# Kernel tuning notes

Hardware: AMD Instinct MI355X
Metric: run time of the kernel (lower is better)

## Reference

```python
import jax, jax.numpy as jnp
import numpy as np

B, T, F = 2, 128, 88          # batch, time frames, pitch bins (hard-coded 88)
HIDDEN = 64                    # LSTM input dim
N_UNIT = 64                    # channel dim (= 2 * lstm hidden 32)
N_HEAD = 4
HEAD_DIM = N_UNIT // N_HEAD    # 16
WINDOW = 7
N_LAYERS = 2
DIFF_STEPS = 100
LSTM_H = N_UNIT // 2           # 32 per direction


def setup_inputs() -> dict:
    key = jax.random.key(0)
    ks = jax.random.split(key, 12)
    s = 0.05
    inp = {
        'x': jax.random.normal(ks[0], (B, T * F, HIDDEN), jnp.float32),
        't': jax.random.randint(ks[1], (B,), 0, DIFF_STEPS, jnp.int32),
        # LSTM params, stacked [layer, direction, ...]; layer-1 input dim == 2*LSTM_H == HIDDEN
        'lstm_w_ih': s * jax.random.normal(ks[2], (N_LAYERS, 2, 4 * LSTM_H, HIDDEN), jnp.float32),
        'lstm_w_hh': s * jax.random.normal(ks[3], (N_LAYERS, 2, 4 * LSTM_H, LSTM_H), jnp.float32),
        'lstm_b_ih': s * jax.random.normal(ks[4], (N_LAYERS, 2, 4 * LSTM_H), jnp.float32),
        'lstm_b_hh': s * jax.random.normal(ks[5], (N_LAYERS, 2, 4 * LSTM_H), jnp.float32),
        # per-NA-layer params
        't_emb': s * jax.random.normal(ks[6], (N_LAYERS, DIFF_STEPS, N_UNIT), jnp.float32),
        'w_qkv': s * jax.random.normal(ks[7], (N_LAYERS, N_UNIT, 3 * N_UNIT), jnp.float32),
        'b_qkv': jnp.zeros((N_LAYERS, 3 * N_UNIT), jnp.float32),
        'rpb': s * jax.random.normal(ks[8], (N_LAYERS, N_HEAD, 2 * WINDOW - 1, 2 * WINDOW - 1), jnp.float32),
        'w_proj': s * jax.random.normal(ks[9], (N_LAYERS, N_UNIT, N_UNIT), jnp.float32),
        'b_proj': jnp.zeros((N_LAYERS, N_UNIT), jnp.float32),
    }
    return inp


def _lstm_dir(x, w_ih, w_hh, b_ih, b_hh, reverse):
    # x: [N, T, D]; pytorch gate order i, f, g, o
    N = x.shape[0]
    H = w_hh.shape[1]
    xs = jnp.swapaxes(x, 0, 1)
    if reverse:
        xs = xs[::-1]
    b = b_ih + b_hh
    def step(carry, xt):
        h, c = carry
        g = xt @ w_ih.T + h @ w_hh.T + b
        i, f, gg, o = jnp.split(g, 4, axis=-1)
        c = jax.nn.sigmoid(f) * c + jax.nn.sigmoid(i) * jnp.tanh(gg)
        h = jax.nn.sigmoid(o) * jnp.tanh(c)
        return (h, c), h
    h0 = jnp.zeros((N, H), x.dtype)
    _, hs = jax.lax.scan(step, (h0, h0), xs)
    if reverse:
        hs = hs[::-1]
    return jnp.swapaxes(hs, 0, 1)


def _bilstm(x, w_ih, w_hh, b_ih, b_hh):
    for l in range(w_ih.shape[0]):
        fwd = _lstm_dir(x, w_ih[l, 0], w_hh[l, 0], b_ih[l, 0], b_hh[l, 0], False)
        bwd = _lstm_dir(x, w_ih[l, 1], w_hh[l, 1], b_ih[l, 1], b_hh[l, 1], True)
        x = jnp.concatenate([fwd, bwd], axis=-1)
    return x


def _nbh(L, w):
    # NATTEN-style clamped (non-shrinking) neighborhood window per axis
    i = jnp.arange(L)
    start = jnp.clip(i - w // 2, 0, L - w)
    idx = start[:, None] + jnp.arange(w)[None, :]   # [L, w] absolute neighbor idx
    rel = idx - i[:, None] + (w - 1)                # [L, w] rel-pos-bias idx in [0, 2w-2]
    return idx, rel


def _na2d(x, t_idx, emb, wqkv, bqkv, rpb_l, wproj, bproj):
    # x: [B, Th, Tw, C]; diffusion-step conditioning via learned embedding add
    Bx, Th, Tw, C = x.shape
    h = x + emb[t_idx][:, None, None, :]
    qkv = (h @ wqkv + bqkv).reshape(Bx, Th, Tw, 3, N_HEAD, HEAD_DIM)
    q = jnp.moveaxis(qkv[..., 0, :, :], 3, 1) * (HEAD_DIM ** -0.5)  # [B,h,Th,Tw,d]
    k = jnp.moveaxis(qkv[..., 1, :, :], 3, 1)
    v = jnp.moveaxis(qkv[..., 2, :, :], 3, 1)
    ih, rh = _nbh(Th, WINDOW)
    iw, rw = _nbh(Tw, WINDOW)
    # gather windowed neighbors: [B,h,Th,Tw,w,w,d]
    kn = k[:, :, ih[:, None, :, None], iw[None, :, None, :], :]
    vn = v[:, :, ih[:, None, :, None], iw[None, :, None, :], :]
    bias = rpb_l[:, rh[:, None, :, None], rw[None, :, None, :]]     # [h,Th,Tw,w,w]
    logits = jnp.einsum('bhijd,bhijkld->bhijkl', q, kn) + bias[None]
    attn = jax.nn.softmax(logits.reshape(Bx, N_HEAD, Th, Tw, -1), axis=-1).reshape(logits.shape)
    out = jnp.einsum('bhijkl,bhijkld->bhijd', attn, vn)             # [B,h,Th,Tw,d]
    out = jnp.moveaxis(out, 1, 3).reshape(Bx, Th, Tw, C)
    return out @ wproj + bproj


def reference(x, t, lstm_w_ih, lstm_w_hh, lstm_b_ih, lstm_b_hh,
              t_emb, w_qkv, b_qkv, rpb, w_proj, b_proj):
    Bx = x.shape[0]
    Hin = x.shape[-1]
    Tt = x.shape[1] // F
    h = x.reshape(Bx, Tt, F, Hin).transpose(0, 2, 1, 3).reshape(Bx * F, Tt, Hin)
    h = _bilstm(h, lstm_w_ih, lstm_w_hh, lstm_b_ih, lstm_b_hh)      # [B*88, T, n_unit]
    # -> [B, T, 88, n_unit] 2D grid (height=T, width=88)
    h = h.reshape(Bx, F, Tt, N_UNIT).transpose(0, 2, 1, 3)
    for l in range(N_LAYERS):
        h = h + _na2d(h, t, t_emb[l], w_qkv[l], b_qkv[l], rpb[l], w_proj[l], b_proj[l])
    return h
```

## Files before the change

kernel.cpp:

```cpp
#include <hip/hip_runtime.h>
#include <math.h>

#define B_ 2
#define T_ 128
#define F_ 88
#define HID 64
#define NU 64
#define NH 4
#define HD 16
#define LH 32
#define NSEQ (B_*F_)
#define NTOK (B_*T_*F_)
#define NPOS (T_*F_)

__device__ __forceinline__ float fsig(float x) {
    return __builtin_amdgcn_rcpf(1.0f + __expf(-x));
}
__device__ __forceinline__ float ftanh(float x) {
    return 2.0f * __builtin_amdgcn_rcpf(1.0f + __expf(-2.0f*x)) - 1.0f;
}
__device__ __forceinline__ float rdlane(float v, int l) {
    return __uint_as_float(__builtin_amdgcn_readlane(__float_as_uint(v), l));
}

template<int LAYER>
__global__ void __launch_bounds__(256, 2) gg_kernel(
    const float* __restrict__ xin,
    const float* __restrict__ w_ih,
    const float* __restrict__ b_ih,
    const float* __restrict__ b_hh,
    float* __restrict__ G)
{
    __shared__ __align__(16) float xts[32][68];
    __shared__ __align__(16) float wsh[256][68];
    __shared__ float bsh[256];
    const int s  = blockIdx.x;
    const int t0 = blockIdx.y * 32;
    const int b = s / F_, f = s % F_;
    const int tid = threadIdx.x;

    for (int n = tid; n < 32*64; n += 256) {
        const int tt = n >> 6, k = n & 63;
        xts[tt][k] = (LAYER == 0)
            ? xin[(((size_t)b*T_ + t0+tt)*F_ + f)*HID + k]
            : xin[((size_t)s*T_ + t0+tt)*HID + k];
    }
    for (int n = tid; n < 256*64; n += 256) {
        const int row = n >> 6, k = n & 63;
        wsh[row][k] = w_ih[((size_t)LAYER*256 + row)*HID + k];
    }
    bsh[tid] = b_ih[LAYER*256 + tid] + b_hh[LAYER*256 + tid];
    __syncthreads();

    const int lane = tid & 63;
    const int g    = tid >> 6;
    const int dir  = g >> 1;
    const int th   = g & 1;
    const int rowA = dir*128 + lane;
    const int rowB = dir*128 + 64 + lane;

    float accA[16] = {}, accB[16] = {};
    #pragma unroll 4
    for (int k4 = 0; k4 < 16; k4++) {
        const float4 wA = *(const float4*)&wsh[rowA][k4*4];
        const float4 wB = *(const float4*)&wsh[rowB][k4*4];
        #pragma unroll
        for (int tt = 0; tt < 16; tt++) {
            const float4 xv = *(const float4*)&xts[th*16+tt][k4*4];
            accA[tt] += wA.x*xv.x + wA.y*xv.y + wA.z*xv.z + wA.w*xv.w;
            accB[tt] += wB.x*xv.x + wB.y*xv.y + wB.z*xv.z + wB.w*xv.w;
        }
    }
    const float bA = bsh[rowA], bB = bsh[rowB];
    float2* gout = (float2*)G + ((size_t)(s*2+dir)*T_ + t0 + th*16)*64 + lane;
    #pragma unroll
    for (int tt = 0; tt < 16; tt++) {
        float2 o; o.x = accA[tt] + bA; o.y = accB[tt] + bB;
        gout[(size_t)tt*64] = o;
    }
}

template<int LAYER>
__global__ void __launch_bounds__(128, 1) lstm_rec(
    const float* __restrict__ G,
    const float* __restrict__ w_hh,
    float* __restrict__ outp)
{
    const int s = blockIdx.x;
    const int b = s / F_, f = s % F_;
    const int lane = threadIdx.x & 63;
    const int dir  = threadIdx.x >> 6;

    float whA[LH], whB[LH];
    {
        const float4* pa = (const float4*)(w_hh + ((size_t)(LAYER*2+dir)*128 + lane)*LH);
        const float4* pb = (const float4*)(w_hh + ((size_t)(LAYER*2+dir)*128 + 64 + lane)*LH);
        #pragma unroll
        for (int k4 = 0; k4 < LH/4; k4++) {
            float4 a = pa[k4], c4 = pb[k4];
            whA[k4*4+0]=a.x;  whA[k4*4+1]=a.y;  whA[k4*4+2]=a.z;  whA[k4*4+3]=a.w;
            whB[k4*4+0]=c4.x; whB[k4*4+1]=c4.y; whB[k4*4+2]=c4.z; whB[k4*4+3]=c4.w;
        }
    }
    const float2* gp = (const float2*)G + (size_t)(s*2+dir)*T_*64 + lane;
    #define GTIME(st) (dir ? (T_-1-(st)) : (st))

    float h = 0.f, c = 0.f;

    #define STEP(gAv, gBv, stepi)                                            \
    {                                                                        \
        float aA0 = (gAv), aB0 = (gBv), aA1 = 0.f, aB1 = 0.f;                \
        _Pragma("unroll")                                                    \
        for (int k = 0; k < 16; k++) {                                       \
            const float hk  = rdlane(h, k);                                  \
            const float hk2 = rdlane(h, k+16);                               \
            aA0 += whA[k]*hk;     aB0 += whB[k]*hk;                          \
            aA1 += whA[k+16]*hk2; aB1 += whB[k+16]*hk2;                      \
        }                                                                    \
        const float accA = aA0 + aA1, accB = aB0 + aB1;                      \
        const float e0 = fsig(accA);                                         \
        const float e1 = (lane < LH) ? ftanh(accB) : fsig(accB);             \
        const float x0 = __shfl_xor(e0, 32, 64);       \
        const float x1 = __shfl_xor(e1, 32, 64);       \
        c = x0*c + e0*e1;                                                    \
        h = x1 * ftanh(c);                                                   \
        if (lane < LH) {                                                     \
            const int tm = GTIME(stepi);                                     \
            if (LAYER == 0)                                                  \
                outp[((size_t)s*T_ + tm)*NU + dir*LH + lane] = h;            \
            else                                                             \
                outp[(((size_t)b*T_ + tm)*F_ + f)*NU + dir*LH + lane] = h;   \
        }                                                                    \
    }

    float2 A[4], Bf[4];
    #pragma unroll
    for (int i = 0; i < 4; i++) A[i]  = gp[(size_t)GTIME(i)*64];
    #pragma unroll
    for (int i = 0; i < 4; i++) Bf[i] = gp[(size_t)GTIME(4+i)*64];

    #pragma unroll 1
    for (int grp = 0; grp < 32; grp++) {
        float2 P[4];
        const int pf = (grp < 30 ? grp + 2 : 31) * 4;
        #pragma unroll
        for (int i = 0; i < 4; i++) P[i] = gp[(size_t)GTIME(pf+i)*64];
        #pragma unroll
        for (int i = 0; i < 4; i++) { STEP(A[i].x, A[i].y, grp*4 + i); }
        #pragma unroll
        for (int i = 0; i < 4; i++) { A[i] = Bf[i]; Bf[i] = P[i]; }
    }
    #undef STEP
    #undef GTIME
}

__global__ void __launch_bounds__(256, 2) qkv_kernel(
    const float* __restrict__ hcur,
    const int*   __restrict__ tarr,
    const float* __restrict__ t_emb,
    const float* __restrict__ w_qkv,
    const float* __restrict__ b_qkv,
    const int layer,
    float* __restrict__ qb, float* __restrict__ kb, float* __restrict__ vb)
{
    __shared__ float as[64][65];
    __shared__ float wsh[64][64];
    const int m0 = blockIdx.x * 64;
    const int which = blockIdx.y;
    const int tid = threadIdx.x;
    const int bidx = m0 / NPOS;
    const int tb = tarr[bidx];
    const float* embp = t_emb + ((size_t)layer*100 + tb)*HID;

    for (int n = tid; n < 64*64; n += 256) {
        const int mm = n >> 6, k = n & 63;
        as[mm][k]  = hcur[((size_t)m0+mm)*64 + k] + embp[k];
        wsh[mm][k] = w_qkv[((size_t)layer*64 + mm)*192 + which*64 + k];
    }
    __syncthreads();

    const int tm = tid >> 4, tn = tid & 15;
    float acc[4][4] = {};
    for (int k = 0; k < 64; k++) {
        const float a0 = as[tm*4+0][k];
        const float a1 = as[tm*4+1][k];
        const float a2 = as[tm*4+2][k];
        const float a3 = as[tm*4+3][k];
        const float4 w = *(const float4*)&wsh[k][tn*4];
        acc[0][0]+=a0*w.x; acc[0][1]+=a0*w.y; acc[0][2]+=a0*w.z; acc[0][3]+=a0*w.w;
        acc[1][0]+=a1*w.x; acc[1][1]+=a1*w.y; acc[1][2]+=a1*w.z; acc[1][3]+=a1*w.w;
        acc[2][0]+=a2*w.x; acc[2][1]+=a2*w.y; acc[2][2]+=a2*w.z; acc[2][3]+=a2*w.w;
        acc[3][0]+=a3*w.x; acc[3][1]+=a3*w.y; acc[3][2]+=a3*w.z; acc[3][3]+=a3*w.w;
    }

    float* dst = (which == 0) ? qb : (which == 1) ? kb : vb;
    const float scale = (which == 0) ? 0.25f : 1.0f;
    const int hh = tn >> 2;
    const int dbase = (tn & 3) * 4;
    const float4 bv = *(const float4*)&b_qkv[(size_t)layer*192 + which*64 + tn*4];
    #pragma unroll
    for (int r = 0; r < 4; r++) {
        const int row = m0 + tm*4 + r;
        const int pos = row - bidx*NPOS;
        float4 o;
        o.x = (acc[r][0] + bv.x) * scale;
        o.y = (acc[r][1] + bv.y) * scale;
        o.z = (acc[r][2] + bv.z) * scale;
        o.w = (acc[r][3] + bv.w) * scale;
        *(float4*)&dst[(((size_t)bidx*NH + hh)*NPOS + pos)*HD + dbase] = o;
    }
}

__global__ void __launch_bounds__(192, 1) nattn_kernel(
    const float* __restrict__ qb,
    const float* __restrict__ kb,
    const float* __restrict__ vb,
    const float* __restrict__ rpb,
    const int layer,
    float* __restrict__ ao)
{
    __shared__ float ks[8][88][20];
    __shared__ float rp[169];
    const int blk = blockIdx.x;
    const int bh = blk & 7;
    const int it = blk >> 3;
    const int i0 = it*2;
    const int h  = bh & 3;
    const int bb = bh >> 2;
    const int tid = threadIdx.x;
    const int rs = min(max(i0-3, 0), T_-8);
    const float* kbase = kb + (size_t)bh*NPOS*HD;
    const float* vbase = vb + (size_t)bh*NPOS*HD;

    const bool act = (tid < 2*F_);
    const int isub = act ? (tid / F_) : 0;
    const int j    = act ? (tid - isub*F_) : 0;
    const int i    = i0 + isub;
    const int ihs  = min(max(i-3, 0), T_-7);
    const int ro   = ihs - rs;
    const int cw   = min(max(j-3, 0), F_-7);

    float4 q0, q1, q2, q3;
    if (act) {
        const float4* qp = (const float4*)&qb[((size_t)bh*NPOS + i*F_ + j)*HD];
        q0 = qp[0]; q1 = qp[1]; q2 = qp[2]; q3 = qp[3];
    }
    for (int n = tid; n < 169; n += 192)
        rp[n] = rpb[((size_t)layer*NH + h)*169 + n];
    for (int n4 = tid; n4 < 8*88*4; n4 += 192) {
        const int d4   = n4 & 3;
        const int rest = n4 >> 2;
        const int c    = rest % 88;
        const int r    = rest / 88;
        *(float4*)&ks[r][c][d4*4] =
            *(const float4*)&kbase[((size_t)(rs+r)*F_ + c)*HD + d4*4];
    }
    __syncthreads();

    float lg[49];
    if (act) {
        #pragma unroll
        for (int ki = 0; ki < 7; ki++) {
            const int rh = ihs + ki - i + 6;
            #pragma unroll
            for (int kj = 0; kj < 7; kj++) {
                const float4* kp = (const float4*)&ks[ro+ki][cw+kj][0];
                const float4 k0 = kp[0], k1 = kp[1], k2 = kp[2], k3 = kp[3];
                float d = q0.x*k0.x + q0.y*k0.y + q0.z*k0.z + q0.w*k0.w
                        + q1.x*k1.x + q1.y*k1.y + q1.z*k1.z + q1.w*k1.w
                        + q2.x*k2.x + q2.y*k2.y + q2.z*k2.z + q2.w*k2.w
                        + q3.x*k3.x + q3.y*k3.y + q3.z*k3.z + q3.w*k3.w;
                lg[ki*7+kj] = d + rp[rh*13 + (cw + kj - j + 6)];
            }
        }
        float m = lg[0];
        #pragma unroll
        for (int n = 1; n < 49; n++) m = fmaxf(m, lg[n]);
        float ssum = 0.f;
        #pragma unroll
        for (int n = 0; n < 49; n++) { lg[n] = __expf(lg[n] - m); ssum += lg[n]; }
        const float inv = __builtin_amdgcn_rcpf(ssum);
        #pragma unroll
        for (int n = 0; n < 49; n++) lg[n] *= inv;
    }
    __syncthreads();
    for (int n4 = tid; n4 < 8*88*4; n4 += 192) {
        const int d4   = n4 & 3;
        const int rest = n4 >> 2;
        const int c    = rest % 88;
        const int r    = rest / 88;
        *(float4*)&ks[r][c][d4*4] =
            *(const float4*)&vbase[((size_t)(rs+r)*F_ + c)*HD + d4*4];
    }
    __syncthreads();
    if (act) {
        float4 o0 = {0,0,0,0}, o1 = {0,0,0,0}, o2 = {0,0,0,0}, o3 = {0,0,0,0};
        #pragma unroll
        for (int ki = 0; ki < 7; ki++) {
            #pragma unroll
            for (int kj = 0; kj < 7; kj++) {
                const float a = lg[ki*7+kj];
                const float4* vp = (const float4*)&ks[ro+ki][cw+kj][0];
                const float4 v0 = vp[0], v1 = vp[1], v2 = vp[2], v3 = vp[3];
                o0.x += a*v0.x; o0.y += a*v0.y; o0.z += a*v0.z; o0.w += a*v0.w;
                o1.x += a*v1.x; o1.y += a*v1.y; o1.z += a*v1.z; o1.w += a*v1.w;
                o2.x += a*v2.x; o2.y += a*v2.y; o2.z += a*v2.z; o2.w += a*v2.w;
                o3.x += a*v3.x; o3.y += a*v3.y; o3.z += a*v3.z; o3.w += a*v3.w;
            }
        }
        float4* op = (float4*)&ao[(((size_t)bb*T_ + i)*F_ + j)*NU + h*HD];
        op[0]=o0; op[1]=o1; op[2]=o2; op[3]=o3;
    }
}

__global__ void __launch_bounds__(256, 2) proj_kernel(
    const float* __restrict__ ain,
    const float* __restrict__ hres,
    const float* __restrict__ w_proj,
    const float* __restrict__ b_proj,
    const int layer,
    float* __restrict__ outp)
{
    __shared__ float as[64][65];
    __shared__ float wsh[64][64];
    const int m0 = blockIdx.x * 64;
    const int tid = threadIdx.x;
    for (int n = tid; n < 64*64; n += 256) {
        const int mm = n >> 6, k = n & 63;
        as[mm][k]  = ain[((size_t)m0+mm)*64 + k];
        wsh[mm][k] = w_proj[(size_t)layer*4096 + n];
    }
    __syncthreads();
    const int tm = tid >> 4, tn = tid & 15;
    float acc[4][4] = {};
    for (int k = 0; k < 64; k++) {
        const float a0 = as[tm*4+0][k];
        const float a1 = as[tm*4+1][k];
        const float a2 = as[tm*4+2][k];
        const float a3 = as[tm*4+3][k];
        const float4 w = *(const float4*)&wsh[k][tn*4];
        acc[0][0]+=a0*w.x; acc[0][1]+=a0*w.y; acc[0][2]+=a0*w.z; acc[0][3]+=a0*w.w;
        acc[1][0]+=a1*w.x; acc[1][1]+=a1*w.y; acc[1][2]+=a1*w.z; acc[1][3]+=a1*w.w;
        acc[2][0]+=a2*w.x; acc[2][1]+=a2*w.y; acc[2][2]+=a2*w.z; acc[2][3]+=a2*w.w;
        acc[3][0]+=a3*w.x; acc[3][1]+=a3*w.y; acc[3][2]+=a3*w.z; acc[3][3]+=a3*w.w;
    }
    const float4 bv = *(const float4*)&b_proj[(size_t)layer*64 + tn*4];
    #pragma unroll
    for (int r = 0; r < 4; r++) {
        const int row = m0 + tm*4 + r;
        const float4 hv = *(const float4*)&hres[(size_t)row*64 + tn*4];
        float4 o;
        o.x = hv.x + acc[r][0] + bv.x;
        o.y = hv.y + acc[r][1] + bv.y;
        o.z = hv.z + acc[r][2] + bv.z;
        o.w = hv.w + acc[r][3] + bv.w;
        *(float4*)&outp[(size_t)row*64 + tn*4] = o;
    }
}

extern "C" void kernel_launch(void* const* d_in, const int* in_sizes, int n_in,
                              void* d_out, int out_size, void* d_ws, size_t ws_size,
                              hipStream_t stream) {
    const float* x      = (const float*)d_in[0];
    const int*   tarr   = (const int*)  d_in[1];
    const float* w_ih   = (const float*)d_in[2];
    const float* w_hh   = (const float*)d_in[3];
    const float* b_ih   = (const float*)d_in[4];
    const float* b_hh   = (const float*)d_in[5];
    const float* t_emb  = (const float*)d_in[6];
    const float* w_qkv  = (const float*)d_in[7];
    const float* b_qkv  = (const float*)d_in[8];
    const float* rpb    = (const float*)d_in[9];
    const float* w_proj = (const float*)d_in[10];
    const float* b_proj = (const float*)d_in[11];

    float* ws   = (float*)d_ws;
    const size_t CH = (size_t)NTOK * NU;
    float* hcur = ws;
    float* h0   = ws + CH;
    float* G    = ws + 2*CH;
    float* qbuf = ws + 2*CH;
    float* kbuf = ws + 3*CH;
    float* vbuf = ws + 4*CH;
    float* ao   = ws + 5*CH;
    float* outp = (float*)d_out;

    gg_kernel<0><<<dim3(NSEQ, T_/32), 256, 0, stream>>>(x,  w_ih, b_ih, b_hh, G);
    lstm_rec<0><<<NSEQ, 128, 0, stream>>>(G, w_hh, h0);
    gg_kernel<1><<<dim3(NSEQ, T_/32), 256, 0, stream>>>(h0, w_ih, b_ih, b_hh, G);
    lstm_rec<1><<<NSEQ, 128, 0, stream>>>(G, w_hh, hcur);

    for (int l = 0; l < 2; l++) {
        qkv_kernel<<<dim3(NTOK/64, 3), 256, 0, stream>>>(
            hcur, tarr, t_emb, w_qkv, b_qkv, l, qbuf, kbuf, vbuf);
        nattn_kernel<<<(T_/2)*8, 192, 0, stream>>>(
            qbuf, kbuf, vbuf, rpb, l, ao);
        proj_kernel<<<NTOK/64, 256, 0, stream>>>(
            ao, hcur, w_proj, b_proj, l, (l == 0) ? hcur : outp);
    }
}
```

Before: 266.4 us.

## Split LSTM directions into separate blocks and stage gate inputs in LDS

```diff
diff --git a/kernel.cpp b/kernel.cpp
--- a/kernel.cpp
+++ b/kernel.cpp
@@ -81,76 +81,80 @@
 }
 
 template<int LAYER>
-__global__ void __launch_bounds__(128, 1) lstm_rec(
+__global__ void __launch_bounds__(64, 1) lstm_rec(
     const float* __restrict__ G,
     const float* __restrict__ w_hh,
     float* __restrict__ outp)
 {
-    const int s = blockIdx.x;
+    __shared__ float2 gsl[T_][64];
+    const int s   = blockIdx.x >> 1;
+    const int dir = blockIdx.x & 1;
     const int b = s / F_, f = s % F_;
-    const int lane = threadIdx.x & 63;
-    const int dir  = threadIdx.x >> 6;
-
-    float whA[LH], whB[LH];
+    const int lane = threadIdx.x;
+
+    float2 wh2[LH];
     {
         const float4* pa = (const float4*)(w_hh + ((size_t)(LAYER*2+dir)*128 + lane)*LH);
         const float4* pb = (const float4*)(w_hh + ((size_t)(LAYER*2+dir)*128 + 64 + lane)*LH);
         #pragma unroll
         for (int k4 = 0; k4 < LH/4; k4++) {
             float4 a = pa[k4], c4 = pb[k4];
-            whA[k4*4+0]=a.x;  whA[k4*4+1]=a.y;  whA[k4*4+2]=a.z;  whA[k4*4+3]=a.w;
-            whB[k4*4+0]=c4.x; whB[k4*4+1]=c4.y; whB[k4*4+2]=c4.z; whB[k4*4+3]=c4.w;
-        }
-    }
-    const float2* gp = (const float2*)G + (size_t)(s*2+dir)*T_*64 + lane;
+            wh2[k4*4+0].x=a.x; wh2[k4*4+0].y=c4.x;
+            wh2[k4*4+1].x=a.y; wh2[k4*4+1].y=c4.y;
+            wh2[k4*4+2].x=a.z; wh2[k4*4+2].y=c4.z;
+            wh2[k4*4+3].x=a.w; wh2[k4*4+3].y=c4.w;
+        }
+    }
+
+    {
+        const float4* g4 = (const float4*)(G + (size_t)(s*2+dir)*T_*128);
+        float4* ls4 = (float4*)&gsl[0][0];
+        #pragma unroll 8
+        for (int it = 0; it < 64; it++)
+            ls4[it*64 + lane] = g4[(size_t)it*64 + lane];
+    }
+    __syncthreads();
+
+    const float a1 = (lane < LH) ? 2.f : 1.f;
+    const float c1 = (lane < LH) ? -1.f : 0.f;
+
+    float h = 0.f, c = 0.f;
     #define GTIME(st) (dir ? (T_-1-(st)) : (st))
 
-    float h = 0.f, c = 0.f;
-
-    #define STEP(gAv, gBv, stepi)                                            \
-    {                                                                        \
-        float aA0 = (gAv), aB0 = (gBv), aA1 = 0.f, aB1 = 0.f;                \
-        _Pragma("unroll")                                                    \
-        for (int k = 0; k < 16; k++) {                                       \
-            const float hk  = rdlane(h, k);                                  \
-            const float hk2 = rdlane(h, k+16);                               \
-            aA0 += whA[k]*hk;     aB0 += whB[k]*hk;                          \
-            aA1 += whA[k+16]*hk2; aB1 += whB[k+16]*hk2;                      \
-        }                                                                    \
-        const float accA = aA0 + aA1, accB = aB0 + aB1;                      \
-        const float e0 = fsig(accA);                                         \
-        const float e1 = (lane < LH) ? ftanh(accB) : fsig(accB);             \
-        const float x0 = __shfl_xor(e0, 32, 64);       \
-        const float x1 = __shfl_xor(e1, 32, 64);       \
-        c = x0*c + e0*e1;                                                    \
-        h = x1 * ftanh(c);                                                   \
-        if (lane < LH) {                                                     \
-            const int tm = GTIME(stepi);                                     \
-            if (LAYER == 0)                                                  \
-                outp[((size_t)s*T_ + tm)*NU + dir*LH + lane] = h;            \
-            else                                                             \
-                outp[(((size_t)b*T_ + tm)*F_ + f)*NU + dir*LH + lane] = h;   \
-        }                                                                    \
-    }
-
-    float2 A[4], Bf[4];
-    #pragma unroll
-    for (int i = 0; i < 4; i++) A[i]  = gp[(size_t)GTIME(i)*64];
-    #pragma unroll
-    for (int i = 0; i < 4; i++) Bf[i] = gp[(size_t)GTIME(4+i)*64];
-
-    #pragma unroll 1
-    for (int grp = 0; grp < 32; grp++) {
-        float2 P[4];
-        const int pf = (grp < 30 ? grp + 2 : 31) * 4;
-        #pragma unroll
-        for (int i = 0; i < 4; i++) P[i] = gp[(size_t)GTIME(pf+i)*64];
-        #pragma unroll
-        for (int i = 0; i < 4; i++) { STEP(A[i].x, A[i].y, grp*4 + i); }
-        #pragma unroll
-        for (int i = 0; i < 4; i++) { A[i] = Bf[i]; Bf[i] = P[i]; }
-    }
-    #undef STEP
+    float2 gcur = gsl[GTIME(0)][lane];
+    float2 gnxt = gsl[GTIME(1)][lane];
+
+    #pragma unroll 4
+    for (int step = 0; step < T_; step++) {
+        const int pf = step + 2 < T_ ? step + 2 : T_ - 1;
+        const float2 gpf = gsl[GTIME(pf)][lane];
+
+        float2 acc0 = gcur, acc1 = {0.f, 0.f};
+        #pragma unroll
+        for (int k = 0; k < 16; k++) {
+            const float hk  = rdlane(h, k);
+            const float hk2 = rdlane(h, k+16);
+            acc0.x += wh2[k].x*hk;     acc0.y += wh2[k].y*hk;
+            acc1.x += wh2[k+16].x*hk2; acc1.y += wh2[k+16].y*hk2;
+        }
+        const float accA = acc0.x + acc1.x;
+        const float accB = acc0.y + acc1.y;
+
+        const float e0 = fsig(accA);
+        const float e1 = fmaf(a1, fsig(a1*accB), c1);
+        const float x0 = __shfl_xor(e0, 32, 64);
+        const float x1 = __shfl_xor(e1, 32, 64);
+        c = x0*c + e0*e1;
+        h = x1 * ftanh(c);
+        if (lane < LH) {
+            const int tm = GTIME(step);
+            if (LAYER == 0)
+                outp[((size_t)s*T_ + tm)*NU + dir*LH + lane] = h;
+            else
+                outp[(((size_t)b*T_ + tm)*F_ + f)*NU + dir*LH + lane] = h;
+        }
+        gcur = gnxt; gnxt = gpf;
+    }
     #undef GTIME
 }
 
@@ -386,9 +390,9 @@
     float* outp = (float*)d_out;
 
     gg_kernel<0><<<dim3(NSEQ, T_/32), 256, 0, stream>>>(x,  w_ih, b_ih, b_hh, G);
-    lstm_rec<0><<<NSEQ, 128, 0, stream>>>(G, w_hh, h0);
+    lstm_rec<0><<<NSEQ*2, 64, 0, stream>>>(G, w_hh, h0);
     gg_kernel<1><<<dim3(NSEQ, T_/32), 256, 0, stream>>>(h0, w_ih, b_ih, b_hh, G);
-    lstm_rec<1><<<NSEQ, 128, 0, stream>>>(G, w_hh, hcur);
+    lstm_rec<1><<<NSEQ*2, 64, 0, stream>>>(G, w_hh, hcur);
 
     for (int l = 0; l < 2; l++) {
         qkv_kernel<<<dim3(NTOK/64, 3), 256, 0, stream>>>(
```

Result: no change. 268.7 us (+0.9%).

## Split LSTM recurrence into one wave per direction with 4-gate lanes and staged output

Applied to the files above, without the earlier changes.

```diff
diff --git a/kernel.cpp b/kernel.cpp
--- a/kernel.cpp
+++ b/kernel.cpp
@@ -72,86 +72,102 @@
         }
     }
     const float bA = bsh[rowA], bB = bsh[rowB];
-    float2* gout = (float2*)G + ((size_t)(s*2+dir)*T_ + t0 + th*16)*64 + lane;
+    float* gbase = G + (((size_t)(s*2+dir)*T_ + t0 + th*16)*LH + (lane & 31))*4
+                     + (lane >> 5)*2;
     #pragma unroll
     for (int tt = 0; tt < 16; tt++) {
         float2 o; o.x = accA[tt] + bA; o.y = accB[tt] + bB;
-        gout[(size_t)tt*64] = o;
+        *(float2*)(gbase + (size_t)tt*128) = o;
     }
 }
 
 template<int LAYER>
-__global__ void __launch_bounds__(128, 1) lstm_rec(
+__global__ void __launch_bounds__(64, 1) lstm_rec(
     const float* __restrict__ G,
     const float* __restrict__ w_hh,
     float* __restrict__ outp)
 {
-    const int s = blockIdx.x;
+    __shared__ float hbuf[T_][LH];
+    const int chain = blockIdx.x;
+    const int s = chain >> 1, dir = chain & 1;
     const int b = s / F_, f = s % F_;
-    const int lane = threadIdx.x & 63;
-    const int dir  = threadIdx.x >> 6;
-
-    float whA[LH], whB[LH];
+    const int lane = threadIdx.x;
+    const int u = lane & 31;
+
+    float wi[LH], wf[LH], wg[LH], wo[LH];
     {
-        const float4* pa = (const float4*)(w_hh + ((size_t)(LAYER*2+dir)*128 + lane)*LH);
-        const float4* pb = (const float4*)(w_hh + ((size_t)(LAYER*2+dir)*128 + 64 + lane)*LH);
+        const float* wb = w_hh + (size_t)((LAYER*2+dir)*128)*LH;
+        const float4* pi = (const float4*)(wb + (size_t)(0*LH + u)*LH);
+        const float4* pf = (const float4*)(wb + (size_t)(1*LH + u)*LH);
+        const float4* pg = (const float4*)(wb + (size_t)(2*LH + u)*LH);
+        const float4* po = (const float4*)(wb + (size_t)(3*LH + u)*LH);
         #pragma unroll
         for (int k4 = 0; k4 < LH/4; k4++) {
-            float4 a = pa[k4], c4 = pb[k4];
-            whA[k4*4+0]=a.x;  whA[k4*4+1]=a.y;  whA[k4*4+2]=a.z;  whA[k4*4+3]=a.w;
-            whB[k4*4+0]=c4.x; whB[k4*4+1]=c4.y; whB[k4*4+2]=c4.z; whB[k4*4+3]=c4.w;
-        }
-    }
-    const float2* gp = (const float2*)G + (size_t)(s*2+dir)*T_*64 + lane;
+            float4 a = pi[k4], bq = pf[k4], cq = pg[k4], dq = po[k4];
+            wi[k4*4+0]=a.x;  wi[k4*4+1]=a.y;  wi[k4*4+2]=a.z;  wi[k4*4+3]=a.w;
+            wf[k4*4+0]=bq.x; wf[k4*4+1]=bq.y; wf[k4*4+2]=bq.z; wf[k4*4+3]=bq.w;
+            wg[k4*4+0]=cq.x; wg[k4*4+1]=cq.y; wg[k4*4+2]=cq.z; wg[k4*4+3]=cq.w;
+            wo[k4*4+0]=dq.x; wo[k4*4+1]=dq.y; wo[k4*4+2]=dq.z; wo[k4*4+3]=dq.w;
+        }
+    }
+    const float4* gp = (const float4*)G + (size_t)chain*T_*LH + u;
     #define GTIME(st) (dir ? (T_-1-(st)) : (st))
 
     float h = 0.f, c = 0.f;
 
-    #define STEP(gAv, gBv, stepi)                                            \
+    #define STEP(g4, stepi)                                                  \
     {                                                                        \
-        float aA0 = (gAv), aB0 = (gBv), aA1 = 0.f, aB1 = 0.f;                \
+        float ci = (g4).x, cg = (g4).y, cf = (g4).z, co = (g4).w;            \
+        float ci1 = 0.f, cg1 = 0.f, cf1 = 0.f, co1 = 0.f;                    \
         _Pragma("unroll")                                                    \
         for (int k = 0; k < 16; k++) {                                       \
             const float hk  = rdlane(h, k);                                  \
             const float hk2 = rdlane(h, k+16);                               \
-            aA0 += whA[k]*hk;     aB0 += whB[k]*hk;                          \
-            aA1 += whA[k+16]*hk2; aB1 += whB[k+16]*hk2;                      \
+            ci  += wi[k]*hk;     cg  += wg[k]*hk;                            \
+            cf  += wf[k]*hk;     co  += wo[k]*hk;                            \
+            ci1 += wi[k+16]*hk2; cg1 += wg[k+16]*hk2;                        \
+            cf1 += wf[k+16]*hk2; co1 += wo[k+16]*hk2;                        \
         }                                                                    \
-        const float accA = aA0 + aA1, accB = aB0 + aB1;                      \
-        const float e0 = fsig(accA);                                         \
-        const float e1 = (lane < LH) ? ftanh(accB) : fsig(accB);             \
-        const float x0 = __shfl_xor(e0, 32, 64);       \
-        const float x1 = __shfl_xor(e1, 32, 64);       \
-        c = x0*c + e0*e1;                                                    \
-        h = x1 * ftanh(c);                                                   \
-        if (lane < LH) {                                                     \
-            const int tm = GTIME(stepi);                                     \
-            if (LAYER == 0)                                                  \
-                outp[((size_t)s*T_ + tm)*NU + dir*LH + lane] = h;            \
-            else                                                             \
-                outp[(((size_t)b*T_ + tm)*F_ + f)*NU + dir*LH + lane] = h;   \
-        }                                                                    \
-    }
-
-    float2 A[4], Bf[4];
+        const float ti = fsig(ci+ci1), tf = fsig(cf+cf1);                    \
+        const float to = fsig(co+co1), tg = ftanh(cg+cg1);                   \
+        c = tf*c + ti*tg;                                                    \
+        h = to * ftanh(c);                                                   \
+        if (lane < LH) hbuf[GTIME(stepi)][u] = h;                            \
+    }
+
+    float4 A[4], Bf[4];
     #pragma unroll
-    for (int i = 0; i < 4; i++) A[i]  = gp[(size_t)GTIME(i)*64];
+    for (int i = 0; i < 4; i++) A[i]  = gp[(size_t)GTIME(i)*LH];
     #pragma unroll
-    for (int i = 0; i < 4; i++) Bf[i] = gp[(size_t)GTIME(4+i)*64];
+    for (int i = 0; i < 4; i++) Bf[i] = gp[(size_t)GTIME(4+i)*LH];
 
     #pragma unroll 1
     for (int grp = 0; grp < 32; grp++) {
-        float2 P[4];
-        const int pf = (grp < 30 ? grp + 2 : 31) * 4;
-        #pragma unroll
-        for (int i = 0; i < 4; i++) P[i] = gp[(size_t)GTIME(pf+i)*64];
-        #pragma unroll
-        for (int i = 0; i < 4; i++) { STEP(A[i].x, A[i].y, grp*4 + i); }
+        float4 P[4];
+        const int pf4 = (grp < 30 ? grp + 2 : 31) * 4;
+        #pragma unroll
+        for (int i = 0; i < 4; i++) P[i] = gp[(size_t)GTIME(pf4+i)*LH];
+        #pragma unroll
+        for (int i = 0; i < 4; i++) { STEP(A[i], grp*4 + i); }
         #pragma unroll
         for (int i = 0; i < 4; i++) { A[i] = Bf[i]; Bf[i] = P[i]; }
     }
     #undef STEP
     #undef GTIME
+    __syncthreads();
+
+    const float4* l4 = (const float4*)&hbuf[0][0];
+    if (LAYER == 0) {
+        for (int idx = lane; idx < T_*8; idx += 64) {
+            const int t = idx >> 3, q = idx & 7;
+            *(float4*)&outp[((size_t)s*T_ + t)*NU + dir*LH + q*4] = l4[idx];
+        }
+    } else {
+        for (int idx = lane; idx < T_*8; idx += 64) {
+            const int t = idx >> 3, q = idx & 7;
+            *(float4*)&outp[(((size_t)b*T_ + t)*F_ + f)*NU + dir*LH + q*4] = l4[idx];
+        }
+    }
 }
 
 __global__ void __launch_bounds__(256, 2) qkv_kernel(
@@ -386,9 +402,9 @@
     float* outp = (float*)d_out;
 
     gg_kernel<0><<<dim3(NSEQ, T_/32), 256, 0, stream>>>(x,  w_ih, b_ih, b_hh, G);
-    lstm_rec<0><<<NSEQ, 128, 0, stream>>>(G, w_hh, h0);
+    lstm_rec<0><<<NSEQ*2, 64, 0, stream>>>(G, w_hh, h0);
     gg_kernel<1><<<dim3(NSEQ, T_/32), 256, 0, stream>>>(h0, w_ih, b_ih, b_hh, G);
-    lstm_rec<1><<<NSEQ, 128, 0, stream>>>(G, w_hh, hcur);
+    lstm_rec<1><<<NSEQ*2, 64, 0, stream>>>(G, w_hh, hcur);
 
     for (int l = 0; l < 2; l++) {
         qkv_kernel<<<dim3(NTOK/64, 3), 256, 0, stream>>>(
```

New measurement: 285.1 us. +7.1%, slower.
